# Kernel tuning notes

Measured on AMD Instinct MI355X. Metric: run time of the kernel, lower is better.

Reference implementation:

```python
import jax, jax.numpy as jnp
import numpy as np

B, S, W, D, H = 2, 2048, 32, 1024, 16

def setup_inputs() -> dict:
    key = jax.random.key(0)
    ks = jax.random.split(key, 8)
    scale = 0.02
    return {
        'q': jax.random.normal(ks[0], (B, S, D), jnp.float32),
        'k': jax.random.normal(ks[1], (B, S, W, D), jnp.float32),
        'v': jax.random.normal(ks[2], (B, S, W, D), jnp.float32),
        'Wq': jax.random.normal(ks[3], (D, D), jnp.float32) * scale,
        'bq': jnp.zeros((D,), jnp.float32),
        'Wk': jax.random.normal(ks[4], (D, D), jnp.float32) * scale,
        'bk': jnp.zeros((D,), jnp.float32),
        'Wv': jax.random.normal(ks[5], (D, D), jnp.float32) * scale,
        'bv': jnp.zeros((D,), jnp.float32),
        'Wo': jax.random.normal(ks[6], (D, D), jnp.float32) * scale,
        'bo': jnp.zeros((D,), jnp.float32),
        'num_heads': H,
    }

def reference(q, k, v, Wq, bq, Wk, bk, Wv, bv, Wo, bo, num_heads):
    b, s, d = q.shape
    w = k.shape[2]
    hd = d // num_heads
    # query: Linear -> view(B,S,H,1,hd) -> transpose(1,2) => (B,H,S,1,hd)
    qh = (q @ Wq.T + bq).reshape(b, s, num_heads, 1, hd).transpose(0, 2, 1, 3, 4)
    # key/value: Linear then RAW view (B,H,S,W,hd) -- faithful to torch .view (no head transpose)
    kh = (k @ Wk.T + bk).reshape(b, num_heads, s, w, hd)
    vh = (v @ Wv.T + bv).reshape(b, num_heads, s, w, hd)
    # scores: (B,H,S,1,W), scaled by sqrt(head_dim) (query.shape[-1] inside attention)
    scores = jnp.einsum('bhsid,bhswd->bhsiw', qh, kh) / jnp.sqrt(jnp.float32(hd))
    # Softmax(dim=1) normalizes over the HEAD axis -- faithful to the original
    attn = jax.nn.softmax(scores, axis=1)
    A = jnp.einsum('bhsiw,bhswd->bhsid', attn, vh)[:, :, :, 0, :]  # (B,H,S,hd)
    out = A.reshape(b, s, d)  # raw view, matches torch .view(B,S,D)
    return out @ Wo.T + bo
```

## Files before the change

kernel.cpp:

```cpp
#include <hip/hip_runtime.h>
#include <hip/hip_bf16.h>


#define DEVI __device__ __forceinline__

typedef __attribute__((ext_vector_type(8))) short bf16x8;
typedef __attribute__((ext_vector_type(4))) float f32x4;
typedef const __attribute__((address_space(1))) void* gvp;
typedef __attribute__((address_space(3))) void* lvp;

DEVI ushort f2bf(float f) {
  uint u = __float_as_uint(f);
  u = u + 0x7fffu + ((u >> 16) & 1u);
  return (ushort)(u >> 16);
}
DEVI float bf2f(ushort u) { return __uint_as_float(((uint)u) << 16); }

__global__ __launch_bounds__(256) void cast_kernel(const float* __restrict__ in,
                                                   ushort* __restrict__ out,
                                                   long n) {
  long i = ((long)blockIdx.x * 256 + threadIdx.x) * 8;
  const long stride = (long)gridDim.x * 256 * 8;
  for (; i < n; i += stride) {
    float4 a = *reinterpret_cast<const float4*>(in + i);
    float4 b = *reinterpret_cast<const float4*>(in + i + 4);
    ushort o[8];
    o[0] = f2bf(a.x); o[1] = f2bf(a.y); o[2] = f2bf(a.z); o[3] = f2bf(a.w);
    o[4] = f2bf(b.x); o[5] = f2bf(b.y); o[6] = f2bf(b.z); o[7] = f2bf(b.w);
    *reinterpret_cast<int4*>(out + i) = *reinterpret_cast<const int4*>(o);
  }
}

template <int FJ0>
DEVI void mfma16b(f32x4 (&acc)[8][4], const bf16x8 (&A)[8], const bf16x8 (&B)[2]) {
  __builtin_amdgcn_s_setprio(1);
#pragma unroll
  for (int fi = 0; fi < 8; ++fi)
#pragma unroll
    for (int j = 0; j < 2; ++j)
      acc[fi][FJ0 + j] = __builtin_amdgcn_mfma_f32_16x16x32_bf16(
          A[fi], B[j], acc[fi][FJ0 + j], 0, 0, 0);
  __builtin_amdgcn_s_setprio(0);
}

__global__ __launch_bounds__(512)
__attribute__((amdgpu_waves_per_eu(2, 2)))
void gemm_big(const float* __restrict__ Ag, const ushort* __restrict__ Wg,
              const float* __restrict__ bias, ushort* __restrict__ Cg) {
  constexpr int K = 1024;
  __shared__ char lds[131072];
  const int tid = threadIdx.x;
  const int lane = tid & 63;
  const int wave = tid >> 6;
  const int wm = wave >> 2;
  const int wn = wave & 3;
  const int d = blockIdx.x;
  const int bn = (d >> 3) & 3;
  const size_t bm = (size_t)(d & 7) * (gridDim.x >> 5) + (d >> 5);

  const ushort* bB = Wg + (size_t)bn * 256 * K;

  const int r0 = tid >> 3;
  const int c0 = (tid & 7) ^ (r0 & 7);
  const float* pR0 = Ag + bm * 256 * K + (size_t)r0 * K + c0 * 8;
  const float* pR1 = pR0 + 64 * K;
  const ushort* bS0 = bB + (size_t)r0 * K + c0 * 8;
  const ushort* bS1 = bB + (size_t)(r0 + 64) * K + c0 * 8;
  const ushort* bS2 = bB + (size_t)(r0 + 128) * K + c0 * 8;
  const ushort* bS3 = bB + (size_t)(r0 + 192) * K + c0 * 8;

  const int lm = lane & 15;
  const int q = lane >> 4;
  const int rowB = lm * 128;
  const int swz0 = (q ^ (lm & 7)) * 16;
  const int swz1 = ((4 + q) ^ (lm & 7)) * 16;
  const char* ldsc = (const char*)lds;
  const char* p0A = ldsc + wm * 16384 + rowB;
  const char* p0B = ldsc + 32768 + (wn >> 1) * 16384 + (wn & 1) * 8192 + rowB;
  const char* p1A = p0A + 65536;
  const char* p1B = p0B + 65536;

  f32x4 acc[8][4] = {};
  bf16x8 A8[8];
  bf16x8 Bf[2];
  float4 sa[8], sb[8];

#define SB0 __builtin_amdgcn_sched_barrier(0)
#define BAR __builtin_amdgcn_s_barrier()
#define STG(p0, p1, ktE, ldsOff)                                                 \
  {                                                                              \
    __builtin_amdgcn_global_load_lds((gvp)((p0) + (ktE)),                        \
                                     (lvp)(lds + (ldsOff) + tid * 16), 16, 0, 0);\
    __builtin_amdgcn_global_load_lds((gvp)((p1) + (ktE)),                        \
                                     (lvp)(lds + (ldsOff) + 8192 + tid * 16),    \
                                     16, 0, 0);                                  \
  }
#define AISS8(set, off)                                                  \
  {                                                                      \
    set[0] = *reinterpret_cast<const float4*>(pR0 + (off));              \
    set[1] = *reinterpret_cast<const float4*>(pR0 + (off) + 4);          \
    set[2] = *reinterpret_cast<const float4*>(pR1 + (off));              \
    set[3] = *reinterpret_cast<const float4*>(pR1 + (off) + 4);          \
    set[4] = *reinterpret_cast<const float4*>(pR0 + 131072 + (off));     \
    set[5] = *reinterpret_cast<const float4*>(pR0 + 131072 + (off) + 4); \
    set[6] = *reinterpret_cast<const float4*>(pR1 + 131072 + (off));     \
    set[7] = *reinterpret_cast<const float4*>(pR1 + 131072 + (off) + 4); \
  }
#define CVTPAIR(v0, v1, dstoff)                                             \
  {                                                                         \
    uint w0, w1, w2, w3;                                                    \
    asm("v_cvt_pk_bf16_f32 %0,%1,%2" : "=v"(w0) : "v"((v0).x), "v"((v0).y)); \
    asm("v_cvt_pk_bf16_f32 %0,%1,%2" : "=v"(w1) : "v"((v0).z), "v"((v0).w)); \
    asm("v_cvt_pk_bf16_f32 %0,%1,%2" : "=v"(w2) : "v"((v1).x), "v"((v1).y)); \
    asm("v_cvt_pk_bf16_f32 %0,%1,%2" : "=v"(w3) : "v"((v1).z), "v"((v1).w)); \
    *reinterpret_cast<uint4*>(lds + (dstoff) + tid * 16) =                  \
        make_uint4(w0, w1, w2, w3);                                         \
  }
#define CVT8(set, base)                 \
  {                                     \
    CVTPAIR(set[0], set[1], (base));    \
    CVTPAIR(set[2], set[3], (base) + 8192);  \
    CVTPAIR(set[4], set[5], (base) + 16384); \
    CVTPAIR(set[6], set[7], (base) + 24576); \
  }
#define PH_SYNC()                                    \
  __builtin_amdgcn_s_barrier();                      \
  asm volatile("s_waitcnt lgkmcnt(0)" ::: "memory"); \
  SB0;
#define LDA8(p, swz)                                                       \
  _Pragma("unroll") for (int i_ = 0; i_ < 8; ++i_) {                       \
    A8[i_] = *reinterpret_cast<const bf16x8*>((p) + i_ * 2048 + (swz));    \
  }
#define LDB2(p, fjb, swz)                                                  \
  {                                                                        \
    Bf[0] = *reinterpret_cast<const bf16x8*>((p) + (fjb) + (swz));         \
    Bf[1] = *reinterpret_cast<const bf16x8*>((p) + (fjb) + 2048 + (swz));  \
  }

  STG(bS0, bS1, 0, 32768); SB0;
  STG(bS2, bS3, 0, 49152); SB0;
  AISS8(sa, 0); SB0;
  AISS8(sb, 64); SB0;
  CVT8(sa, 0);
  CVT8(sb, 65536);
  asm volatile("s_waitcnt vmcnt(0)" ::: "memory");
  asm volatile("s_waitcnt lgkmcnt(0)" ::: "memory");
  BAR;
  SB0;

#define ITER(M)                                                           \
  {                                                                       \
    const int ktB1 = (2 * it + 1) * 64;                                   \
    const int ktB2 = (2 * it + 2) * 64;                                   \
    const int ktA2 = (2 * it + 2) * 64;                                   \
    const int ktA3 = (2 * it + 3) * 64;                                   \
                                                  \
    LDA8(p0A, swz0); LDB2(p0B, 0, swz0);                                  \
    STG(bS0, bS1, ktB1, 98304);                                           \
    PH_SYNC(); mfma16b<0>(acc, A8, Bf); BAR;                              \
                              \
    LDB2(p0B, 4096, swz0);                                                \
    if (M == 0) { AISS8(sa, ktA2); }                                      \
    STG(bS2, bS3, ktB1, 114688);                                          \
    PH_SYNC(); mfma16b<2>(acc, A8, Bf); BAR;                              \
                   \
    LDA8(p0A, swz1); LDB2(p0B, 0, swz1);                                  \
    PH_SYNC(); mfma16b<0>(acc, A8, Bf); BAR;                              \
             \
    LDB2(p0B, 4096, swz1);                                                \
    if (M == 0) { CVT8(sa, 0); }                                          \
    PH_SYNC(); mfma16b<2>(acc, A8, Bf);                                   \
    SB0;                                                                  \
    asm volatile("s_waitcnt vmcnt(0)" ::: "memory");                      \
    BAR; SB0;                                                             \
                                                  \
    LDA8(p1A, swz0); LDB2(p1B, 0, swz0);                                  \
    if (M == 0) STG(bS0, bS1, ktB2, 32768);                               \
    PH_SYNC(); mfma16b<0>(acc, A8, Bf); BAR;                              \
                              \
    LDB2(p1B, 4096, swz0);                                                \
    if (M == 0) { AISS8(sb, ktA3); STG(bS2, bS3, ktB2, 49152); }          \
    PH_SYNC(); mfma16b<2>(acc, A8, Bf); BAR;                              \
                   \
    LDA8(p1A, swz1); LDB2(p1B, 0, swz1);                                  \
    PH_SYNC(); mfma16b<0>(acc, A8, Bf); BAR;                              \
             \
    LDB2(p1B, 4096, swz1);                                                \
    if (M == 0) { CVT8(sb, 65536); }                                      \
    PH_SYNC(); mfma16b<2>(acc, A8, Bf);                                   \
    if (M == 0) {                                                         \
      SB0;                                                                \
      asm volatile("s_waitcnt vmcnt(0)" ::: "memory");                    \
      BAR; SB0;                                                           \
    }                                                                     \
  }

#pragma unroll 1
  for (int it = 0; it < 7; ++it) ITER(0);
  { const int it = 7; ITER(1); }
#undef ITER
#undef STG
#undef AISS8
#undef CVTPAIR
#undef CVT8
#undef PH_SYNC
#undef LDA8
#undef LDB2
#undef SB0
#undef BAR

#pragma unroll
  for (int fi = 0; fi < 8; ++fi) {
#pragma unroll
    for (int fj = 0; fj < 4; ++fj) {
      int n = bn * 256 + wn * 64 + fj * 16 + lm;
      float bv = bias[n];
#pragma unroll
      for (int r = 0; r < 4; ++r) {
        size_t m = bm * 256 + wm * 128 + fi * 16 + ((lane >> 4) * 4) + r;
        Cg[m * 1024 + n] = f2bf(acc[fi][fj][r] + bv);
      }
    }
  }
}

template <typename TOUT>
__global__ __launch_bounds__(256) void gemm_lds(const ushort* __restrict__ Ag,
                                                const ushort* __restrict__ Wg,
                                                const float* __restrict__ bias,
                                                TOUT* __restrict__ Cg) {
  constexpr int K = 1024;
  __shared__ ushort lA[128 * 64];
  __shared__ ushort lB[128 * 64];
  const int tid = threadIdx.x;
  const int lane = tid & 63;
  const int wave = tid >> 6;
  const int wr = (wave >> 1) * 64;
  const int wc = (wave & 1) * 64;
  const int d = blockIdx.x;
  const int bn = (d >> 3) & 7;
  const size_t bm = (size_t)(d & 7) * (gridDim.x >> 6) + (d >> 6);

  const ushort* aB = Ag + bm * 128 * K;
  const ushort* bB = Wg + (size_t)bn * 128 * K;
  const int srow = wave * 32 + (lane >> 3);
  const int scol = ((lane & 7) ^ (lane >> 3)) * 8;
  char* lAc = (char*)lA;
  char* lBc = (char*)lB;

  f32x4 acc[4][4] = {};

  for (int kt = 0; kt < K; kt += 64) {
    __syncthreads();
#pragma unroll
    for (int c = 0; c < 4; ++c) {
      __builtin_amdgcn_global_load_lds(
          (gvp)(aB + (size_t)(srow + c * 8) * K + kt + scol),
          (lvp)(lAc + wave * 4096 + c * 1024), 16, 0, 0);
      __builtin_amdgcn_global_load_lds(
          (gvp)(bB + (size_t)(srow + c * 8) * K + kt + scol),
          (lvp)(lBc + wave * 4096 + c * 1024), 16, 0, 0);
    }
    __syncthreads();
#pragma unroll
    for (int kk = 0; kk < 2; ++kk) {
      bf16x8 af[4], bg[4];
#pragma unroll
      for (int fi = 0; fi < 4; ++fi) {
        int r = wr + fi * 16 + (lane & 15);
        int byte = (r * 128 + kk * 64 + ((lane >> 4) * 16)) ^ ((r & 7) << 4);
        af[fi] = *reinterpret_cast<const bf16x8*>(lAc + byte);
      }
#pragma unroll
      for (int fj = 0; fj < 4; ++fj) {
        int r = wc + fj * 16 + (lane & 15);
        int byte = (r * 128 + kk * 64 + ((lane >> 4) * 16)) ^ ((r & 7) << 4);
        bg[fj] = *reinterpret_cast<const bf16x8*>(lBc + byte);
      }
#pragma unroll
      for (int fi = 0; fi < 4; ++fi)
#pragma unroll
        for (int fj = 0; fj < 4; ++fj)
          acc[fi][fj] = __builtin_amdgcn_mfma_f32_16x16x32_bf16(af[fi], bg[fj],
                                                                acc[fi][fj], 0, 0, 0);
    }
  }
#pragma unroll
  for (int fi = 0; fi < 4; ++fi) {
#pragma unroll
    for (int fj = 0; fj < 4; ++fj) {
      int n = bn * 128 + wc + fj * 16 + (lane & 15);
      float bv = bias[n];
#pragma unroll
      for (int r = 0; r < 4; ++r) {
        size_t m = bm * 128 + wr + fi * 16 + ((lane >> 4) * 4) + r;
        float val = acc[fi][fj][r] + bv;
        if constexpr (sizeof(TOUT) == 2)
          reinterpret_cast<ushort*>(Cg)[m * 1024 + n] = f2bf(val);
        else
          reinterpret_cast<float*>(Cg)[m * 1024 + n] = val;
      }
    }
  }
}

template <typename TIN, typename TOUT>
__global__ __launch_bounds__(256) void gemm_bias(const TIN* __restrict__ Ag,
                                                 const float* __restrict__ Wg,
                                                 const float* __restrict__ bias,
                                                 TOUT* __restrict__ Cg) {
  constexpr int K = 1024;
  __shared__ char lA[128 * 64 * 2];
  __shared__ char lB[128 * 64 * 2];
  const int tid = threadIdx.x;
  const int lane = tid & 63;
  const int wave = tid >> 6;
  const int wr = (wave >> 1) * 64;
  const int wc = (wave & 1) * 64;
  const int bn = blockIdx.x;
  const size_t bm = blockIdx.y;

  const TIN* aBase = Ag + bm * 128 * K;
  const float* bBase = Wg + (size_t)bn * 128 * K;

  f32x4 acc[4][4] = {};

  for (int kt = 0; kt < K; kt += 64) {
    __syncthreads();
    if constexpr (sizeof(TIN) == 4) {
#pragma unroll
      for (int i = 0; i < 8; ++i) {
        int f = tid + i * 256;
        int row = f >> 4, c4 = f & 15;
        const float4 v = *reinterpret_cast<const float4*>(
            reinterpret_cast<const float*>(aBase) + (size_t)row * K + kt + c4 * 4);
        ushort4 pk;
        pk.x = f2bf(v.x); pk.y = f2bf(v.y); pk.z = f2bf(v.z); pk.w = f2bf(v.w);
        int byte = (row * 128 + c4 * 8) ^ ((row & 7) << 4);
        *reinterpret_cast<ushort4*>(lA + byte) = pk;
      }
    } else {
#pragma unroll
      for (int i = 0; i < 4; ++i) {
        int f = tid + i * 256;
        int row = f >> 3, c8 = f & 7;
        int4 v = *reinterpret_cast<const int4*>(
            reinterpret_cast<const ushort*>(aBase) + (size_t)row * K + kt + c8 * 8);
        int byte = (row * 128 + c8 * 16) ^ ((row & 7) << 4);
        *reinterpret_cast<int4*>(lA + byte) = v;
      }
    }
#pragma unroll
    for (int i = 0; i < 8; ++i) {
      int f = tid + i * 256;
      int row = f >> 4, c4 = f & 15;
      const float4 v =
          *reinterpret_cast<const float4*>(bBase + (size_t)row * K + kt + c4 * 4);
      ushort4 pk;
      pk.x = f2bf(v.x); pk.y = f2bf(v.y); pk.z = f2bf(v.z); pk.w = f2bf(v.w);
      int byte = (row * 128 + c4 * 8) ^ ((row & 7) << 4);
      *reinterpret_cast<ushort4*>(lB + byte) = pk;
    }
    __syncthreads();
#pragma unroll
    for (int kk = 0; kk < 2; ++kk) {
      bf16x8 af[4], bg[4];
#pragma unroll
      for (int fi = 0; fi < 4; ++fi) {
        int r = wr + fi * 16 + (lane & 15);
        int byte = (r * 128 + kk * 64 + ((lane >> 4) * 16)) ^ ((r & 7) << 4);
        af[fi] = *reinterpret_cast<const bf16x8*>(lA + byte);
      }
#pragma unroll
      for (int fj = 0; fj < 4; ++fj) {
        int r = wc + fj * 16 + (lane & 15);
        int byte = (r * 128 + kk * 64 + ((lane >> 4) * 16)) ^ ((r & 7) << 4);
        bg[fj] = *reinterpret_cast<const bf16x8*>(lB + byte);
      }
#pragma unroll
      for (int fi = 0; fi < 4; ++fi)
#pragma unroll
        for (int fj = 0; fj < 4; ++fj)
          acc[fi][fj] =
              __builtin_amdgcn_mfma_f32_16x16x32_bf16(af[fi], bg[fj], acc[fi][fj], 0, 0, 0);
    }
  }
#pragma unroll
  for (int fi = 0; fi < 4; ++fi) {
#pragma unroll
    for (int fj = 0; fj < 4; ++fj) {
      int n = bn * 128 + wc + fj * 16 + (lane & 15);
      float bv = bias[n];
#pragma unroll
      for (int r = 0; r < 4; ++r) {
        size_t m = bm * 128 + wr + fi * 16 + ((lane >> 4) * 4) + r;
        float val = acc[fi][fj][r] + bv;
        if constexpr (sizeof(TOUT) == 2)
          reinterpret_cast<ushort*>(Cg)[m * 1024 + n] = f2bf(val);
        else
          reinterpret_cast<float*>(Cg)[m * 1024 + n] = val;
      }
    }
  }
}

__global__ __launch_bounds__(512) void attn_kernel(const ushort* __restrict__ Q,
                                                   const ushort* __restrict__ Kl,
                                                   const ushort* __restrict__ Vl,
                                                   ushort* __restrict__ Aout) {
  const int bs = blockIdx.x;
  const int b = bs >> 11, sp = bs & 2047;
  const int tid = threadIdx.x;
  const int wave = tid >> 6, lane = tid & 63;

  __shared__ ushort qrow[1024];
  __shared__ float sc[16][32];
  __shared__ float attnw[16][32];
  __shared__ float mx[32], rinv[32];

  reinterpret_cast<uint*>(qrow)[tid] =
      reinterpret_cast<const uint*>(Q + (size_t)bs * 1024)[tid];
  __syncthreads();

  const int wp = lane & 31, half = lane >> 5;
#pragma unroll
  for (int hh = 0; hh < 2; ++hh) {
    const int h = wave * 2 + hh;
    const int s_k = h * 128 + (sp >> 4);
    const int w_k = (sp & 15) * 2 + (wp >> 4);
    const ushort* kp =
        Kl + (((size_t)(b * 2048 + s_k) * 32) + w_k) * 1024 + (wp & 15) * 64 + half * 32;
    const ushort* qp = qrow + h * 64 + half * 32;
    float dot = 0.f;
#pragma unroll
    for (int j = 0; j < 32; j += 8) {
      int4 kv = *reinterpret_cast<const int4*>(kp + j);
      int4 qv = *reinterpret_cast<const int4*>(qp + j);
      const ushort* ka = reinterpret_cast<const ushort*>(&kv);
      const ushort* qa = reinterpret_cast<const ushort*>(&qv);
#pragma unroll
      for (int t = 0; t < 8; ++t) dot += bf2f(ka[t]) * bf2f(qa[t]);
    }
    dot += __shfl_xor(dot, 32);
    if (half == 0) sc[h][wp] = dot * 0.125f;
  }
  __syncthreads();
  if (tid < 32) {
    float m = sc[0][tid];
#pragma unroll
    for (int h = 1; h < 16; ++h) m = fmaxf(m, sc[h][tid]);
    float s = 0.f;
#pragma unroll
    for (int h = 0; h < 16; ++h) s += __expf(sc[h][tid] - m);
    mx[tid] = m;
    rinv[tid] = 1.f / s;
  }
  __syncthreads();
  if (lane < 32) {
#pragma unroll
    for (int hh = 0; hh < 2; ++hh) {
      const int h = wave * 2 + hh;
      attnw[h][lane] = __expf(sc[h][lane] - mx[lane]) * rinv[lane];
    }
  }
  __syncthreads();
#pragma unroll
  for (int hh = 0; hh < 2; ++hh) {
    const int h = wave * 2 + hh;
    const int s_k = h * 128 + (sp >> 4);
    const size_t vb = (((size_t)(b * 2048 + s_k) * 32) + (sp & 15) * 2) * 1024;
    float a = 0.f;
#pragma unroll
    for (int w2 = 0; w2 < 32; ++w2) {
      float wgt = attnw[h][w2];
      a += wgt * bf2f(Vl[vb + (size_t)(w2 >> 4) * 1024 + (w2 & 15) * 64 + lane]);
    }
    Aout[(((size_t)(b * 16 + h)) * 2048 + sp) * 64 + lane] = f2bf(a);
  }
}

extern "C" void kernel_launch(void* const* d_in, const int* in_sizes, int n_in,
                              void* d_out, int out_size, void* d_ws, size_t ws_size,
                              hipStream_t stream) {
  const float* q = (const float*)d_in[0];
  const float* k = (const float*)d_in[1];
  const float* v = (const float*)d_in[2];
  const float* Wq = (const float*)d_in[3];
  const float* bq = (const float*)d_in[4];
  const float* Wk = (const float*)d_in[5];
  const float* bk = (const float*)d_in[6];
  const float* Wv = (const float*)d_in[7];
  const float* bv = (const float*)d_in[8];
  const float* Wo = (const float*)d_in[9];
  const float* bo = (const float*)d_in[10];
  float* out = (float*)d_out;

  char* ws = (char*)d_ws;
  const size_t MB = 1u << 20;
  ushort* Qlin = (ushort*)ws;
  ushort* Aws  = (ushort*)(ws + 8 * MB);
  ushort* wkbf = (ushort*)(ws + 16 * MB);
  ushort* wvbf = (ushort*)(ws + 18 * MB);
  ushort* wqbf = (ushort*)(ws + 20 * MB);
  ushort* wobf = (ushort*)(ws + 22 * MB);
  ushort* qbf  = (ushort*)(ws + 24 * MB);
  ushort* Klin = (ushort*)(ws + 32 * MB);
  ushort* Vlin = (ushort*)(ws + 288 * MB);
  const bool full = ws_size >= 800 * MB;

  if (full) {
    cast_kernel<<<dim3(512), 256, 0, stream>>>(Wq, wqbf, 1048576L);
    cast_kernel<<<dim3(512), 256, 0, stream>>>(Wk, wkbf, 1048576L);
    cast_kernel<<<dim3(512), 256, 0, stream>>>(Wv, wvbf, 1048576L);
    cast_kernel<<<dim3(512), 256, 0, stream>>>(Wo, wobf, 1048576L);
    cast_kernel<<<dim3(2048), 256, 0, stream>>>(q, qbf, 4194304L);
    gemm_lds<ushort><<<dim3(256), 256, 0, stream>>>(qbf, wqbf, bq, Qlin);
    gemm_big<<<dim3(2048), 512, 0, stream>>>(k, wkbf, bk, Klin);
    gemm_big<<<dim3(2048), 512, 0, stream>>>(v, wvbf, bv, Vlin);
    attn_kernel<<<dim3(4096), dim3(512), 0, stream>>>(Qlin, Klin, Vlin, Aws);
    gemm_lds<float><<<dim3(256), 256, 0, stream>>>(Aws, wobf, bo, out);
  } else {
    gemm_bias<float, ushort><<<dim3(8, 32), 256, 0, stream>>>(q, Wq, bq, Qlin);
    gemm_bias<float, ushort><<<dim3(8, 1024), 256, 0, stream>>>(k, Wk, bk, Klin);
    gemm_bias<float, ushort><<<dim3(8, 1024), 256, 0, stream>>>(v, Wv, bv, Vlin);
    attn_kernel<<<dim3(4096), dim3(512), 0, stream>>>(Qlin, Klin, Vlin, Aws);
    gemm_bias<ushort, float><<<dim3(8, 32), 256, 0, stream>>>(Aws, Wo, bo, out);
  }
}
```

Baseline: 969.8 us.

## Single staging register set for fp32 A tiles and relax vmcnt waits

New measurement: 913.7 us. -5.8%, faster.

```diff
diff --git a/kernel.cpp b/kernel.cpp
--- a/kernel.cpp
+++ b/kernel.cpp
@@ -83,7 +83,7 @@
   f32x4 acc[8][4] = {};
   bf16x8 A8[8];
   bf16x8 Bf[2];
-  float4 sa[8], sb[8];
+  float4 st[8];
 
 #define SB0 __builtin_amdgcn_sched_barrier(0)
 #define BAR __builtin_amdgcn_s_barrier()
@@ -95,33 +95,33 @@
                                      (lvp)(lds + (ldsOff) + 8192 + tid * 16),    \
                                      16, 0, 0);                                  \
   }
-#define AISS8(set, off)                                                  \
-  {                                                                      \
-    set[0] = *reinterpret_cast<const float4*>(pR0 + (off));              \
-    set[1] = *reinterpret_cast<const float4*>(pR0 + (off) + 4);          \
-    set[2] = *reinterpret_cast<const float4*>(pR1 + (off));              \
-    set[3] = *reinterpret_cast<const float4*>(pR1 + (off) + 4);          \
-    set[4] = *reinterpret_cast<const float4*>(pR0 + 131072 + (off));     \
-    set[5] = *reinterpret_cast<const float4*>(pR0 + 131072 + (off) + 4); \
-    set[6] = *reinterpret_cast<const float4*>(pR1 + 131072 + (off));     \
-    set[7] = *reinterpret_cast<const float4*>(pR1 + 131072 + (off) + 4); \
-  }
-#define CVTPAIR(v0, v1, dstoff)                                             \
-  {                                                                         \
-    uint w0, w1, w2, w3;                                                    \
+#define AISS8(off)                                                      \
+  {                                                                     \
+    st[0] = *reinterpret_cast<const float4*>(pR0 + (off));              \
+    st[1] = *reinterpret_cast<const float4*>(pR0 + (off) + 4);          \
+    st[2] = *reinterpret_cast<const float4*>(pR1 + (off));              \
+    st[3] = *reinterpret_cast<const float4*>(pR1 + (off) + 4);          \
+    st[4] = *reinterpret_cast<const float4*>(pR0 + 131072 + (off));     \
+    st[5] = *reinterpret_cast<const float4*>(pR0 + 131072 + (off) + 4); \
+    st[6] = *reinterpret_cast<const float4*>(pR1 + 131072 + (off));     \
+    st[7] = *reinterpret_cast<const float4*>(pR1 + 131072 + (off) + 4); \
+  }
+#define CVTPAIR(v0, v1, dstoff)                                              \
+  {                                                                          \
+    uint w0, w1, w2, w3;                                                     \
     asm("v_cvt_pk_bf16_f32 %0,%1,%2" : "=v"(w0) : "v"((v0).x), "v"((v0).y)); \
     asm("v_cvt_pk_bf16_f32 %0,%1,%2" : "=v"(w1) : "v"((v0).z), "v"((v0).w)); \
     asm("v_cvt_pk_bf16_f32 %0,%1,%2" : "=v"(w2) : "v"((v1).x), "v"((v1).y)); \
     asm("v_cvt_pk_bf16_f32 %0,%1,%2" : "=v"(w3) : "v"((v1).z), "v"((v1).w)); \
-    *reinterpret_cast<uint4*>(lds + (dstoff) + tid * 16) =                  \
-        make_uint4(w0, w1, w2, w3);                                         \
-  }
-#define CVT8(set, base)                 \
-  {                                     \
-    CVTPAIR(set[0], set[1], (base));    \
-    CVTPAIR(set[2], set[3], (base) + 8192);  \
-    CVTPAIR(set[4], set[5], (base) + 16384); \
-    CVTPAIR(set[6], set[7], (base) + 24576); \
+    *reinterpret_cast<uint4*>(lds + (dstoff) + tid * 16) =                   \
+        make_uint4(w0, w1, w2, w3);                                          \
+  }
+#define CVT8(base)                          \
+  {                                         \
+    CVTPAIR(st[0], st[1], (base));          \
+    CVTPAIR(st[2], st[3], (base) + 8192);   \
+    CVTPAIR(st[4], st[5], (base) + 16384);  \
+    CVTPAIR(st[6], st[7], (base) + 24576);  \
   }
 #define PH_SYNC()                                    \
   __builtin_amdgcn_s_barrier();                      \
@@ -137,13 +137,12 @@
     Bf[1] = *reinterpret_cast<const bf16x8*>((p) + (fjb) + 2048 + (swz));  \
   }
 
-  STG(bS0, bS1, 0, 32768); SB0;
-  STG(bS2, bS3, 0, 49152); SB0;
-  AISS8(sa, 0); SB0;
-  AISS8(sb, 64); SB0;
-  CVT8(sa, 0);
-  CVT8(sb, 65536);
-  asm volatile("s_waitcnt vmcnt(0)" ::: "memory");
+  AISS8(0); SB0;
+  CVT8(0);
+  SB0;
+  STG(bS0, bS1, 0, 32768); STG(bS2, bS3, 0, 49152); SB0;
+  AISS8(64); SB0;
+  asm volatile("s_waitcnt vmcnt(8)" ::: "memory");
   asm volatile("s_waitcnt lgkmcnt(0)" ::: "memory");
   BAR;
   SB0;
@@ -154,43 +153,43 @@
     const int ktB2 = (2 * it + 2) * 64;                                   \
     const int ktA2 = (2 * it + 2) * 64;                                   \
     const int ktA3 = (2 * it + 3) * 64;                                   \
+              \
+    LDA8(p0A, swz0); LDB2(p0B, 0, swz0);                                  \
+    STG(bS0, bS1, ktB1, 98304); STG(bS2, bS3, ktB1, 114688);              \
+    PH_SYNC(); mfma16b<0>(acc, A8, Bf); BAR;                              \
+        \
+    LDB2(p0B, 4096, swz0);                                                \
+    CVT8(65536);                                                          \
+    SB0;                                                                  \
+    if (M == 0) { AISS8(ktA2); SB0; }                                     \
+    PH_SYNC(); mfma16b<2>(acc, A8, Bf); BAR;                              \
                                                   \
-    LDA8(p0A, swz0); LDB2(p0B, 0, swz0);                                  \
-    STG(bS0, bS1, ktB1, 98304);                                           \
-    PH_SYNC(); mfma16b<0>(acc, A8, Bf); BAR;                              \
-                              \
-    LDB2(p0B, 4096, swz0);                                                \
-    if (M == 0) { AISS8(sa, ktA2); }                                      \
-    STG(bS2, bS3, ktB1, 114688);                                          \
-    PH_SYNC(); mfma16b<2>(acc, A8, Bf); BAR;                              \
-                   \
     LDA8(p0A, swz1); LDB2(p0B, 0, swz1);                                  \
     PH_SYNC(); mfma16b<0>(acc, A8, Bf); BAR;                              \
-             \
+                   \
     LDB2(p0B, 4096, swz1);                                                \
-    if (M == 0) { CVT8(sa, 0); }                                          \
     PH_SYNC(); mfma16b<2>(acc, A8, Bf);                                   \
     SB0;                                                                  \
-    asm volatile("s_waitcnt vmcnt(0)" ::: "memory");                      \
+    if (M == 0) { asm volatile("s_waitcnt vmcnt(8)" ::: "memory"); }      \
+    else        { asm volatile("s_waitcnt vmcnt(0)" ::: "memory"); }      \
     BAR; SB0;                                                             \
+              \
+    LDA8(p1A, swz0); LDB2(p1B, 0, swz0);                                  \
+    if (M == 0) { STG(bS0, bS1, ktB2, 32768); STG(bS2, bS3, ktB2, 49152); } \
+    PH_SYNC(); mfma16b<0>(acc, A8, Bf); BAR;                              \
+        \
+    LDB2(p1B, 4096, swz0);                                                \
+    if (M == 0) { CVT8(0); SB0; AISS8(ktA3); SB0; }                       \
+    PH_SYNC(); mfma16b<2>(acc, A8, Bf); BAR;                              \
                                                   \
-    LDA8(p1A, swz0); LDB2(p1B, 0, swz0);                                  \
-    if (M == 0) STG(bS0, bS1, ktB2, 32768);                               \
-    PH_SYNC(); mfma16b<0>(acc, A8, Bf); BAR;                              \
-                              \
-    LDB2(p1B, 4096, swz0);                                                \
-    if (M == 0) { AISS8(sb, ktA3); STG(bS2, bS3, ktB2, 49152); }          \
-    PH_SYNC(); mfma16b<2>(acc, A8, Bf); BAR;                              \
-                   \
     LDA8(p1A, swz1); LDB2(p1B, 0, swz1);                                  \
     PH_SYNC(); mfma16b<0>(acc, A8, Bf); BAR;                              \
-             \
+                   \
     LDB2(p1B, 4096, swz1);                                                \
-    if (M == 0) { CVT8(sb, 65536); }                                      \
     PH_SYNC(); mfma16b<2>(acc, A8, Bf);                                   \
     if (M == 0) {                                                         \
       SB0;                                                                \
-      asm volatile("s_waitcnt vmcnt(0)" ::: "memory");                    \
+      asm volatile("s_waitcnt vmcnt(8)" ::: "memory");                    \
       BAR; SB0;                                                           \
     }                                                                     \
   }
```
